# Kernel optimization log

Hardware: AMD Instinct MI355X
Metric: run time of the kernel (lower is better)

Reference implementation:

```python
import jax, jax.numpy as jnp
import numpy as np

B, S, D = 2, 2048, 4096
QH, KVH = 32, 8
HD = D // QH          # 128
KVD = KVH * HD        # 1024
GROUP = QH // KVH     # 4


def _make_freqs_cis(seq, hd):
    inv = 1.0 / (10000.0 ** (jnp.arange(0, hd, 2, dtype=jnp.float32) / hd))
    ang = jnp.outer(jnp.arange(seq, dtype=jnp.float32), inv)  # [S, HD//2]
    return jnp.stack([jnp.cos(ang), jnp.sin(ang)], axis=-1)    # [S, HD//2, 2]


def setup_inputs() -> dict:
    key = jax.random.key(0)
    ks = jax.random.split(key, 10)
    std = 0.02
    return {
        "xs": jax.random.normal(ks[0], (B, S, D), jnp.float32),
        "startpos": 0,
        "freqs_cis": _make_freqs_cis(S, HD),
        "Wq": jax.random.normal(ks[1], (D, D), jnp.float32) * std,
        "bq": jnp.zeros((D,), jnp.float32),
        "Wk": jax.random.normal(ks[2], (KVD, D), jnp.float32) * std,
        "bk": jnp.zeros((KVD,), jnp.float32),
        "Wv": jax.random.normal(ks[3], (KVD, D), jnp.float32) * std,
        "bv": jnp.zeros((KVD,), jnp.float32),
        "Wo": jax.random.normal(ks[4], (D, D), jnp.float32) * std,
        "bo": jnp.zeros((D,), jnp.float32),
    }


def _apply_rope(x, fc):
    # x: [B,S,H,HD], fc: [S, HD//2, 2] (cos,sin) -> complex multiply per pair
    xr = x.reshape(*x.shape[:-1], HD // 2, 2)
    cos = fc[None, :, None, :, 0]
    sin = fc[None, :, None, :, 1]
    out_r = xr[..., 0] * cos - xr[..., 1] * sin
    out_i = xr[..., 0] * sin + xr[..., 1] * cos
    return jnp.stack([out_r, out_i], axis=-1).reshape(x.shape)


def reference(xs, startpos, freqs_cis, Wq, bq, Wk, bk, Wv, bv, Wo, bo):
    b, s, _ = xs.shape
    q = (xs @ Wq.T + bq).reshape(b, s, QH, HD)
    k = (xs @ Wk.T + bk).reshape(b, s, KVH, HD)
    v = (xs @ Wv.T + bv).reshape(b, s, KVH, HD)

    fc = freqs_cis[startpos:startpos + s]
    q = _apply_rope(q, fc)
    k = _apply_rope(k, fc)
    # startpos == 0: cache write-then-read is identity on current k/v

    # GQA: group q heads per kv head; avoid materializing repeated K/V
    qg = q.transpose(0, 2, 1, 3).reshape(b, KVH, GROUP, s, HD)  # [b,kvh,g,s,d]
    kk = k.transpose(0, 2, 1, 3)                                 # [b,kvh,t,d]
    vv = v.transpose(0, 2, 1, 3)

    scale = 1.0 / jnp.sqrt(jnp.float32(HD))
    logits = jnp.einsum('bhgsd,bhtd->bhgst', qg, kk) * scale
    causal = jnp.tril(jnp.ones((s, s), dtype=bool))
    logits = jnp.where(causal[None, None, None], logits, jnp.float32(-1e30))
    probs = jax.nn.softmax(logits, axis=-1)
    ctx = jnp.einsum('bhgst,bhtd->bhgsd', probs, vv)             # [b,kvh,g,s,d]

    ctx = ctx.reshape(b, QH, s, HD).transpose(0, 2, 1, 3).reshape(b, s, D)
    return ctx @ Wo.T + bo
```

## Files before the change

### kernel.cpp

```cpp
#include <hip/hip_runtime.h>
#include <hip/hip_bf16.h>

typedef __bf16 bf16x8 __attribute__((ext_vector_type(8)));
typedef float  f32x4  __attribute__((ext_vector_type(4)));

#define MFMA(a, b, c) __builtin_amdgcn_mfma_f32_16x16x32_bf16((a), (b), (c), 0, 0, 0)

typedef __attribute__((address_space(1))) void* as1_vp;
typedef __attribute__((address_space(3))) void* as3_vp;

__device__ __forceinline__ void g2lds16(const void* g, void* lds) {
  __builtin_amdgcn_global_load_lds((as1_vp)(unsigned long long)g,
                                   (as3_vp)(unsigned int)(unsigned long long)lds,
                                   16, 0, 0);
}

__device__ __forceinline__ unsigned short bfbits(float x) {
  return __builtin_bit_cast(unsigned short, __float2bfloat16(x));
}

__global__ void cvt_f32_bf16(const float* __restrict__ in,
                             __hip_bfloat16* __restrict__ out, int n4) {
  int i = blockIdx.x * blockDim.x + threadIdx.x;
  if (i >= n4) return;
  float4 v = ((const float4*)in)[i];
  ushort4 u;
  u.x = bfbits(v.x); u.y = bfbits(v.y); u.z = bfbits(v.z); u.w = bfbits(v.w);
  ((ushort4*)out)[i] = u;
}

__global__ void concat_bias(const float* __restrict__ bq, const float* __restrict__ bk,
                            const float* __restrict__ bv, float* __restrict__ out) {
  int i = blockIdx.x * 256 + threadIdx.x;
  float v = (i < 4096) ? bq[i] : ((i < 5120) ? bk[i - 4096] : bv[i - 5120]);
  out[i] = v;
}

__global__ void rope_inplace(__hip_bfloat16* __restrict__ x, const float* __restrict__ fc,
                             const int* __restrict__ startpos, int pitch, int wshift,
                             long npairs) {
  long i = (long)blockIdx.x * blockDim.x + threadIdx.x;
  if (i >= npairs) return;
  int  wi    = (int)(i & ((1 << wshift) - 1));
  long token = i >> wshift;
  int  s  = (int)(token & 2047);
  int  j  = wi & 63;
  int  sp = startpos[0] + s;
  float c  = fc[(sp << 7) + (j << 1)];
  float sn = fc[(sp << 7) + (j << 1) + 1];
  long base = token * pitch + wi * 2;
  float xr = __bfloat162float(x[base]);
  float xi = __bfloat162float(x[base + 1]);
  x[base]     = __float2bfloat16(xr * c - xi * sn);
  x[base + 1] = __float2bfloat16(xr * sn + xi * c);
}

__global__ void transpose_v(const __hip_bfloat16* __restrict__ QKV,
                            __hip_bfloat16* __restrict__ VT) {
  __shared__ __hip_bfloat16 tile[32][33];
  int z = blockIdx.z, b = z >> 3, kvh = z & 7;
  int s0 = blockIdx.x * 32, h0 = blockIdx.y * 32;
  int tx = threadIdx.x, ty = threadIdx.y;
#pragma unroll
  for (int ry = ty; ry < 32; ry += 8)
    tile[ry][tx] =
        QKV[(long)(b * 2048 + s0 + ry) * 6144 + 5120 + kvh * 128 + h0 + tx];
  __syncthreads();
#pragma unroll
  for (int ry = ty; ry < 32; ry += 8)
    VT[((long)z * 128 + h0 + ry) * 2048 + s0 + tx] = tile[tx][ry];
}

#define BAR()  __builtin_amdgcn_s_barrier()
#define SB0()  __builtin_amdgcn_sched_barrier(0)
#define LGK0() do { asm volatile("s_waitcnt lgkmcnt(0)" ::: "memory"); \
                    __builtin_amdgcn_sched_barrier(0); } while (0)
#define VMC8() asm volatile("s_waitcnt vmcnt(8)" ::: "memory")
#define VMC4() asm volatile("s_waitcnt vmcnt(4)" ::: "memory")
#define VMC0() asm volatile("s_waitcnt vmcnt(0)" ::: "memory")
#define PRI1() __builtin_amdgcn_s_setprio(1)
#define PRI0() __builtin_amdgcn_s_setprio(0)

template <int OUT_F32>
__global__ void __launch_bounds__(512, 2)
gemm256_bt(const __hip_bfloat16* __restrict__ A,
           const __hip_bfloat16* __restrict__ W,
           const float* __restrict__ bias,
           void* __restrict__ Cout, int M, int N, int K) {
  __shared__ __align__(16) char smem[131072];
  (void)M;
  const int t = threadIdx.x, w = t >> 6, l = t & 63, quad = l >> 4, lan = l & 15;
  const int wm = w >> 2, wn = w & 3;

  const int nwg = gridDim.x;
  const int xcd = blockIdx.x & 7, lid = blockIdx.x >> 3;
  const int qq = nwg >> 3, rr = nwg & 7;
  const int wg = (xcd < rr ? xcd * (qq + 1) : rr * (qq + 1) + (xcd - rr) * qq) + lid;
  const int ntn = N >> 8;
  const int bm = (wg / ntn) << 8, bn = (wg % ntn) << 8;

  const int csrc = ((t & 3) ^ ((t >> 3) & 3)) << 4;
  const char* aS0 = (const char*)(A + (long)(bm + (t >> 2)) * K) + csrc;
  const char* aS1 = aS0 + (long)K * 256;
  const char* bS0 = (const char*)(W + (long)(bn + (t >> 2)) * K) + csrc;
  const char* bS1 = bS0 + (long)K * 256;
  char* dA0 = smem + (w << 10);
  char* dA1 = smem + 16384 + (w << 10);
  char* dB0 = smem + 32768 + (w << 10);
  char* dB1 = smem + 49152 + (w << 10);

#define STG(src, dst, kt, bb)                                    \
  g2lds16((src) + (kt) * 128, (dst) + (bb) * 65536);             \
  g2lds16((src) + (kt) * 128 + 64, (dst) + (bb) * 65536 + 8192);

  const int rsw = (quad ^ ((lan >> 1) & 3)) << 4;
  const char* aR = smem + wm * 16384 + (lan << 6) + rsw;
  const char* bR = smem + 32768 + (wn >> 1) * 16384 + ((((wn & 1) << 6) + lan) << 6) + rsw;

  f32x4 acc[8][4] = {};
  bf16x8 fA[4][2], fB0[2][2], fB1[2][2];

#define RD_A(mb, bb)                                                          \
  _Pragma("unroll") for (int mm = 0; mm < 4; ++mm)                            \
  _Pragma("unroll") for (int j = 0; j < 2; ++j)                               \
    fA[mm][j] = *(const bf16x8*)(aR + (bb) * 65536 + ((mb) + mm) * 1024 + j * 8192);
#define RD_B(arr, nb, bb)                                                     \
  _Pragma("unroll") for (int nn = 0; nn < 2; ++nn)                            \
  _Pragma("unroll") for (int j = 0; j < 2; ++j)                               \
    arr[nn][j] = *(const bf16x8*)(bR + (bb) * 65536 + ((nb) + nn) * 1024 + j * 8192);
#define MM16(mb, arr, nb)                                                     \
  _Pragma("unroll") for (int mm = 0; mm < 4; ++mm)                            \
  _Pragma("unroll") for (int nn = 0; nn < 2; ++nn)                            \
  _Pragma("unroll") for (int j = 0; j < 2; ++j)                               \
    acc[(mb) + mm][(nb) + nn] = MFMA(fA[mm][j], arr[nn][j], acc[(mb) + mm][(nb) + nn]);

  STG(aS0, dA0, 0, 0); STG(aS1, dA1, 0, 0);
  STG(bS0, dB0, 0, 0); STG(bS1, dB1, 0, 0);
  STG(bS0, dB0, 1, 1); STG(bS1, dB1, 1, 1);
  VMC4();
  BAR();

  const int NT = K >> 6;
  for (int i = 0; i < (NT >> 1) - 1; ++i) {
    const int t0 = i << 1;
    RD_A(0, 0); RD_B(fB0, 0, 0);
    STG(aS0, dA0, t0 + 1, 1);
    SB0(); BAR(); LGK0();
    PRI1(); MM16(0, fB0, 0); PRI0();
    BAR();
    RD_B(fB1, 2, 0);
    STG(aS1, dA1, t0 + 1, 1);
    SB0(); BAR(); LGK0();
    PRI1(); MM16(0, fB1, 2); PRI0();
    BAR();
    RD_A(4, 0);
    STG(bS0, dB0, t0 + 2, 0);
    SB0(); BAR(); LGK0();
    PRI1(); MM16(4, fB0, 0); PRI0();
    BAR();
    STG(bS1, dB1, t0 + 2, 0);
    SB0(); BAR();
    PRI1(); MM16(4, fB1, 2); PRI0();
    VMC4();
    BAR();
    RD_A(0, 1); RD_B(fB0, 0, 1);
    STG(aS0, dA0, t0 + 2, 0);
    SB0(); BAR(); LGK0();
    PRI1(); MM16(0, fB0, 0); PRI0();
    BAR();
    RD_B(fB1, 2, 1);
    STG(aS1, dA1, t0 + 2, 0);
    SB0(); BAR(); LGK0();
    PRI1(); MM16(0, fB1, 2); PRI0();
    BAR();
    RD_A(4, 1);
    STG(bS0, dB0, t0 + 3, 1);
    SB0(); BAR(); LGK0();
    PRI1(); MM16(4, fB0, 0); PRI0();
    BAR();
    STG(bS1, dB1, t0 + 3, 1);
    SB0(); BAR();
    PRI1(); MM16(4, fB1, 2); PRI0();
    VMC4();
    BAR();
  }

  {
    RD_A(0, 0); RD_B(fB0, 0, 0);
    STG(aS0, dA0, NT - 1, 1);
    SB0(); BAR(); LGK0();
    PRI1(); MM16(0, fB0, 0); PRI0();
    BAR();
    RD_B(fB1, 2, 0);
    STG(aS1, dA1, NT - 1, 1);
    SB0(); BAR(); LGK0();
    PRI1(); MM16(0, fB1, 2); PRI0();
    BAR();
    RD_A(4, 0);
    SB0(); BAR(); LGK0();
    PRI1(); MM16(4, fB0, 0); PRI0();
    BAR();
    BAR();
    PRI1(); MM16(4, fB1, 2); PRI0();
    VMC0();
    BAR();
    RD_A(0, 1); RD_B(fB0, 0, 1);
    SB0(); BAR(); LGK0();
    PRI1(); MM16(0, fB0, 0); PRI0();
    BAR();
    RD_B(fB1, 2, 1);
    SB0(); BAR(); LGK0();
    PRI1(); MM16(0, fB1, 2); PRI0();
    BAR();
    RD_A(4, 1);
    SB0(); BAR(); LGK0();
    PRI1(); MM16(4, fB0, 0); PRI0();
    BAR();
    PRI1(); MM16(4, fB1, 2); PRI0();
  }

  float bsv[4];
#pragma unroll
  for (int n = 0; n < 4; ++n) bsv[n] = bias[bn + (wn << 6) + (n << 4) + lan];
#pragma unroll
  for (int m = 0; m < 8; ++m) {
#pragma unroll
    for (int e = 0; e < 4; ++e) {
      const long row = bm + (wm << 7) + (m << 4) + (quad << 2) + e;
#pragma unroll
      for (int n = 0; n < 4; ++n) {
        const float v = acc[m][n][e] + bsv[n];
        const long col = bn + (wn << 6) + (n << 4) + lan;
        if (OUT_F32) ((float*)Cout)[row * N + col] = v;
        else ((__hip_bfloat16*)Cout)[row * N + col] = __float2bfloat16(v);
      }
    }
  }
}
#undef STG
#undef RD_A
#undef RD_B
#undef MM16

__global__ void __launch_bounds__(256, 2) flash_attn(const __hip_bfloat16* __restrict__ QKV,
                                                     const __hip_bfloat16* __restrict__ VT,
                                                     __hip_bfloat16* __restrict__ Ctx, int S) {
  __shared__ __align__(16) char smem[66560];
  char* Ks0 = smem;
  char* Ks1 = smem + 16384;
  char* Vs  = smem + 32768;
  char* Ps  = smem + 49152;
  const int t = threadIdx.x, w = t >> 6, l = t & 63, quad = l >> 4, lan = l & 15;
  const int b = blockIdx.z, qh = blockIdx.y, kvh = qh >> 2;
  const int q0idx = (int)gridDim.x - 1 - blockIdx.x;
  const int q0 = q0idx << 7;
  const float cl = 0.08838834764831845f * 1.4426950408889634f;

  {
    int rl = l >> 4, cd = l & 15;
#pragma unroll
    for (int ii = 0; ii < 8; ii++) {
      int i = (w << 3) + ii;
      int r = (i << 2) + rl;
      int cs = cd ^ (r & 15);
      const char* g =
          (const char*)(QKV + (long)(b * S + q0 + r) * 6144 + qh * 128) + (cs << 4);
      g2lds16(g, smem + (i << 10));
    }
  }
  __syncthreads();
  bf16x8 qf[2][4];
#pragma unroll
  for (int st = 0; st < 2; st++) {
    int row = ((((w << 1) + st) << 4) + lan);
#pragma unroll
    for (int ks = 0; ks < 4; ks++)
      qf[st][ks] = *(const bf16x8*)(smem + (row << 8) + ((((ks << 2) + quad) ^ lan) << 4));
  }
  __syncthreads();

  const int ntiles = (q0idx << 1) + 2;

  auto stageK = [&](int kt, char* dst) {
    int rl = l >> 4, cd = l & 15;
#pragma unroll
    for (int ii = 0; ii < 4; ii++) {
      int i = (w << 2) + ii;
      int r = (i << 2) + rl;
      int cs = cd ^ (r & 15);
      const char* g =
          (const char*)(QKV + (long)(b * S + (kt << 6) + r) * 6144 + 4096 + kvh * 128) +
          (cs << 4);
      g2lds16(g, dst + (i << 10));
    }
  };
  auto stageV = [&](int kt) {
    int dl = l >> 3, cd2 = l & 7;
#pragma unroll
    for (int ii = 0; ii < 4; ii++) {
      int i = (w << 2) + ii;
      int d = (i << 3) + dl;
      int cs = cd2 ^ dl;
      const char* g =
          (const char*)(VT + ((long)((b << 3) + kvh) * 128 + d) * S + (kt << 6)) + (cs << 4);
      g2lds16(g, Vs + (i << 10));
    }
  };

  f32x4 o[2][8] = {};
  float m0[2] = {-__builtin_inff(), -__builtin_inff()};
  float lsum[2] = {0.f, 0.f};

  stageK(0, Ks0);

  for (int kt = 0; kt < ntiles; kt++) {
    const int t0 = kt << 6;
    char* Kcur = (kt & 1) ? Ks1 : Ks0;
    char* Knxt = (kt & 1) ? Ks0 : Ks1;
    SB0(); BAR();
    stageV(kt);
    const int tn = (kt + 1 < ntiles) ? kt + 1 : kt;
    stageK(tn, Knxt);
    VMC8();
    SB0(); BAR();

    f32x4 sa[2][4] = {{}, {}};
    PRI1();
#pragma unroll
    for (int j = 0; j < 4; j++)
#pragma unroll
      for (int ks = 0; ks < 4; ks++) {
        bf16x8 kf = *(const bf16x8*)(Kcur + (((j << 4) + lan) << 8) +
                                     ((((ks << 2) + quad) ^ lan) << 4));
        sa[0][j] = MFMA(kf, qf[0][ks], sa[0][j]);
        sa[1][j] = MFMA(kf, qf[1][ks], sa[1][j]);
      }
    PRI0();

#pragma unroll
    for (int st = 0; st < 2; st++) {
      const int strip = (w << 1) + st;
      const int qg = q0 + (strip << 4) + lan;
      if (t0 + 63 > q0 + (strip << 4)) {
#pragma unroll
        for (int j = 0; j < 4; j++)
#pragma unroll
          for (int e = 0; e < 4; e++)
            if (t0 + (j << 4) + (quad << 2) + e > qg) sa[st][j][e] = -1e30f;
      }
      float mq = sa[st][0][0];
#pragma unroll
      for (int j = 0; j < 4; j++)
#pragma unroll
        for (int e = 0; e < 4; e++) mq = fmaxf(mq, sa[st][j][e]);
      mq = fmaxf(mq, __shfl_xor(mq, 16));
      mq = fmaxf(mq, __shfl_xor(mq, 32));
      float mn = fmaxf(m0[st], mq);
      float al = exp2f((m0[st] - mn) * cl);
      m0[st] = mn;
      float rs = 0.f;
      char* prow = Ps + strip * 2176 + lan * 136;
#pragma unroll
      for (int j = 0; j < 4; j++) {
        float p0 = exp2f((sa[st][j][0] - mn) * cl);
        float p1 = exp2f((sa[st][j][1] - mn) * cl);
        float p2 = exp2f((sa[st][j][2] - mn) * cl);
        float p3 = exp2f((sa[st][j][3] - mn) * cl);
        rs += (p0 + p1) + (p2 + p3);
        ushort4 u;
        u.x = bfbits(p0); u.y = bfbits(p1); u.z = bfbits(p2); u.w = bfbits(p3);
        *(ushort4*)(prow + (j << 5) + (quad << 3)) = u;
      }
      rs += __shfl_xor(rs, 16);
      rs += __shfl_xor(rs, 32);
      lsum[st] = lsum[st] * al + rs;
#pragma unroll
      for (int dt = 0; dt < 8; dt++) o[st][dt] *= al;
    }

    bf16x8 pf[2][2];
#pragma unroll
    for (int st = 0; st < 2; st++) {
      char* prow = Ps + ((w << 1) + st) * 2176 + lan * 136;
      pf[st][0] = *(const bf16x8*)(prow + (quad << 4));
      pf[st][1] = *(const bf16x8*)(prow + 64 + (quad << 4));
    }

    VMC4();
    SB0(); BAR();

    PRI1();
#pragma unroll
    for (int dt = 0; dt < 8; dt++) {
      const int drow = (dt << 4) + lan;
#pragma unroll
      for (int ks = 0; ks < 2; ks++) {
        bf16x8 vf = *(const bf16x8*)(Vs + (drow << 7) +
                                     ((((ks << 2) + quad) ^ (lan & 7)) << 4));
        o[0][dt] = MFMA(vf, pf[0][ks], o[0][dt]);
        o[1][dt] = MFMA(vf, pf[1][ks], o[1][dt]);
      }
    }
    PRI0();
  }

#pragma unroll
  for (int st = 0; st < 2; st++) {
    float inv = 1.0f / lsum[st];
    int strip = (w << 1) + st;
    long token = (long)b * S + q0 + (strip << 4) + lan;
    __hip_bfloat16* obase = Ctx + token * 4096 + qh * 128;
#pragma unroll
    for (int dt = 0; dt < 8; dt++) {
      ushort4 u;
      u.x = bfbits(o[st][dt][0] * inv);
      u.y = bfbits(o[st][dt][1] * inv);
      u.z = bfbits(o[st][dt][2] * inv);
      u.w = bfbits(o[st][dt][3] * inv);
      *(ushort4*)(obase + (dt << 4) + (quad << 2)) = u;
    }
  }
}

extern "C" void kernel_launch(void* const* d_in, const int* in_sizes, int n_in,
                              void* d_out, int out_size, void* d_ws, size_t ws_size,
                              hipStream_t stream) {
  const float* xs = (const float*)d_in[0];
  const int* startpos = (const int*)d_in[1];
  const float* fc = (const float*)d_in[2];
  const float* Wq = (const float*)d_in[3];
  const float* bq = (const float*)d_in[4];
  const float* Wk = (const float*)d_in[5];
  const float* bk = (const float*)d_in[6];
  const float* Wv = (const float*)d_in[7];
  const float* bv = (const float*)d_in[8];
  const float* Wo = (const float*)d_in[9];
  const float* bo = (const float*)d_in[10];
  float* out = (float*)d_out;
  char* ws = (char*)d_ws;

  __hip_bfloat16* Wqkvb = (__hip_bfloat16*)(ws);
  __hip_bfloat16* Xb    = (__hip_bfloat16*)(ws + 50331648L);
  __hip_bfloat16* QKVb  = (__hip_bfloat16*)(ws + 83886080L);
  __hip_bfloat16* VbT   = (__hip_bfloat16*)(ws + 134217728L);
  float*          bqkv  = (float*)(ws + 142606336L);
  __hip_bfloat16* Wob   = Wqkvb;
  __hip_bfloat16* Ctx   = Xb;

  cvt_f32_bf16<<<16384, 256, 0, stream>>>(xs, Xb, 4194304);
  cvt_f32_bf16<<<16384, 256, 0, stream>>>(Wq, Wqkvb, 4194304);
  cvt_f32_bf16<<<4096, 256, 0, stream>>>(Wk, Wqkvb + 16777216L, 1048576);
  cvt_f32_bf16<<<4096, 256, 0, stream>>>(Wv, Wqkvb + 20971520L, 1048576);
  concat_bias<<<24, 256, 0, stream>>>(bq, bk, bv, bqkv);

  gemm256_bt<0><<<dim3(384), 512, 0, stream>>>(Xb, Wqkvb, bqkv, QKVb, 4096, 6144, 4096);

  rope_inplace<<<32768, 256, 0, stream>>>(QKVb, fc, startpos, 6144, 11, 8388608L);
  rope_inplace<<<8192, 256, 0, stream>>>(QKVb + 4096, fc, startpos, 6144, 9, 2097152L);
  transpose_v<<<dim3(64, 4, 16), dim3(32, 8), 0, stream>>>(QKVb, VbT);
  cvt_f32_bf16<<<16384, 256, 0, stream>>>(Wo, Wob, 4194304);

  flash_attn<<<dim3(16, 32, 2), 256, 0, stream>>>(QKVb, VbT, Ctx, 2048);

  gemm256_bt<1><<<dim3(256), 512, 0, stream>>>(Ctx, Wob, bo, out, 4096, 4096, 4096);
}
```

Measured before the change: 808.9 us.

## Keep softmax probabilities in registers for PV MFMA and add lazy rescaling

The P tile no longer round-trips through LDS. The probabilities stay in registers as bf16 packs and feed 16x16x16 MFMAs directly, with V^T pre-permuted in the transpose kernel so its LDS fragment layout matches the score accumulator layout. The online-softmax rescale of the output and row sum is skipped unless the running max grows past a threshold, and bf16 packing uses v_cvt_pk_bf16_f32. This removes LDS writes and reads, and cuts LDS from 66560 to 49152 bytes, at the cost of twice as many smaller MFMAs for PV and a looser softmax max bound.

```diff
diff --git a/kernel.cpp b/kernel.cpp
--- a/kernel.cpp
+++ b/kernel.cpp
@@ -3,8 +3,10 @@
 
 typedef __bf16 bf16x8 __attribute__((ext_vector_type(8)));
 typedef float  f32x4  __attribute__((ext_vector_type(4)));
+typedef short  s16x4  __attribute__((ext_vector_type(4)));
 
 #define MFMA(a, b, c) __builtin_amdgcn_mfma_f32_16x16x32_bf16((a), (b), (c), 0, 0, 0)
+#define MFMA16(a, b, c) __builtin_amdgcn_mfma_f32_16x16x16bf16_1k((a), (b), (c), 0, 0, 0)
 
 typedef __attribute__((address_space(1))) void* as1_vp;
 typedef __attribute__((address_space(3))) void* as3_vp;
@@ -17,6 +19,12 @@
 
 __device__ __forceinline__ unsigned short bfbits(float x) {
   return __builtin_bit_cast(unsigned short, __float2bfloat16(x));
+}
+
+__device__ __forceinline__ unsigned cvtpk(float a, float b) {
+  unsigned r;
+  asm("v_cvt_pk_bf16_f32 %0, %1, %2" : "=v"(r) : "v"(a), "v"(b));
+  return r;
 }
 
 __global__ void cvt_f32_bf16(const float* __restrict__ in,
@@ -24,9 +32,10 @@
   int i = blockIdx.x * blockDim.x + threadIdx.x;
   if (i >= n4) return;
   float4 v = ((const float4*)in)[i];
-  ushort4 u;
-  u.x = bfbits(v.x); u.y = bfbits(v.y); u.z = bfbits(v.z); u.w = bfbits(v.w);
-  ((ushort4*)out)[i] = u;
+  uint2 u;
+  u.x = cvtpk(v.x, v.y);
+  u.y = cvtpk(v.z, v.w);
+  ((uint2*)out)[i] = u;
 }
 
 __global__ void concat_bias(const float* __restrict__ bq, const float* __restrict__ bk,
@@ -67,8 +76,11 @@
         QKV[(long)(b * 2048 + s0 + ry) * 6144 + 5120 + kvh * 128 + h0 + tx];
   __syncthreads();
 #pragma unroll
-  for (int ry = ty; ry < 32; ry += 8)
-    VT[((long)z * 128 + h0 + ry) * 2048 + s0 + tx] = tile[tx][ry];
+  for (int ry = ty; ry < 32; ry += 8) {
+    int dd = h0 + ry;
+    int tc = (s0 + tx) ^ (((dd >> 3) & 1) << 2);
+    VT[((long)z * 128 + dd) * 2048 + tc] = tile[tx][ry];
+  }
 }
 
 #define BAR()  __builtin_amdgcn_s_barrier()
@@ -245,11 +257,10 @@
 __global__ void __launch_bounds__(256, 2) flash_attn(const __hip_bfloat16* __restrict__ QKV,
                                                      const __hip_bfloat16* __restrict__ VT,
                                                      __hip_bfloat16* __restrict__ Ctx, int S) {
-  __shared__ __align__(16) char smem[66560];
+  __shared__ __align__(16) char smem[49152];
   char* Ks0 = smem;
   char* Ks1 = smem + 16384;
   char* Vs  = smem + 32768;
-  char* Ps  = smem + 49152;
   const int t = threadIdx.x, w = t >> 6, l = t & 63, quad = l >> 4, lan = l & 15;
   const int b = blockIdx.z, qh = blockIdx.y, kvh = qh >> 2;
   const int q0idx = (int)gridDim.x - 1 - blockIdx.x;
@@ -310,6 +321,9 @@
   f32x4 o[2][8] = {};
   float m0[2] = {-__builtin_inff(), -__builtin_inff()};
   float lsum[2] = {0.f, 0.f};
+
+  const int l7 = lan & 7;
+  const int hb = (quad & 1) ^ ((lan >> 3) & 1);
 
   stageK(0, Ks0);
 
@@ -337,6 +351,7 @@
       }
     PRI0();
 
+    s16x4 pb[2][4];
 #pragma unroll
     for (int st = 0; st < 2; st++) {
       const int strip = (w << 1) + st;
@@ -355,35 +370,31 @@
         for (int e = 0; e < 4; e++) mq = fmaxf(mq, sa[st][j][e]);
       mq = fmaxf(mq, __shfl_xor(mq, 16));
       mq = fmaxf(mq, __shfl_xor(mq, 32));
-      float mn = fmaxf(m0[st], mq);
-      float al = exp2f((m0[st] - mn) * cl);
-      m0[st] = mn;
+      if (__any(mq > m0[st] + 62.0f)) {
+        float mn = fmaxf(m0[st], mq);
+        float al = exp2f((m0[st] - mn) * cl);
+        m0[st] = mn;
+        lsum[st] *= al;
+#pragma unroll
+        for (int dt = 0; dt < 8; dt++) o[st][dt] *= al;
+      }
+      float nm = -m0[st] * cl;
       float rs = 0.f;
-      char* prow = Ps + strip * 2176 + lan * 136;
 #pragma unroll
       for (int j = 0; j < 4; j++) {
-        float p0 = exp2f((sa[st][j][0] - mn) * cl);
-        float p1 = exp2f((sa[st][j][1] - mn) * cl);
-        float p2 = exp2f((sa[st][j][2] - mn) * cl);
-        float p3 = exp2f((sa[st][j][3] - mn) * cl);
+        float p0 = exp2f(fmaf(sa[st][j][0], cl, nm));
+        float p1 = exp2f(fmaf(sa[st][j][1], cl, nm));
+        float p2 = exp2f(fmaf(sa[st][j][2], cl, nm));
+        float p3 = exp2f(fmaf(sa[st][j][3], cl, nm));
         rs += (p0 + p1) + (p2 + p3);
-        ushort4 u;
-        u.x = bfbits(p0); u.y = bfbits(p1); u.z = bfbits(p2); u.w = bfbits(p3);
-        *(ushort4*)(prow + (j << 5) + (quad << 3)) = u;
+        uint2 up;
+        up.x = cvtpk(p0, p1);
+        up.y = cvtpk(p2, p3);
+        pb[st][j] = __builtin_bit_cast(s16x4, up);
       }
       rs += __shfl_xor(rs, 16);
       rs += __shfl_xor(rs, 32);
-      lsum[st] = lsum[st] * al + rs;
-#pragma unroll
-      for (int dt = 0; dt < 8; dt++) o[st][dt] *= al;
-    }
-
-    bf16x8 pf[2][2];
-#pragma unroll
-    for (int st = 0; st < 2; st++) {
-      char* prow = Ps + ((w << 1) + st) * 2176 + lan * 136;
-      pf[st][0] = *(const bf16x8*)(prow + (quad << 4));
-      pf[st][1] = *(const bf16x8*)(prow + 64 + (quad << 4));
+      lsum[st] += rs;
     }
 
     VMC4();
@@ -393,12 +404,12 @@
 #pragma unroll
     for (int dt = 0; dt < 8; dt++) {
       const int drow = (dt << 4) + lan;
-#pragma unroll
-      for (int ks = 0; ks < 2; ks++) {
-        bf16x8 vf = *(const bf16x8*)(Vs + (drow << 7) +
-                                     ((((ks << 2) + quad) ^ (lan & 7)) << 4));
-        o[0][dt] = MFMA(vf, pf[0][ks], o[0][dt]);
-        o[1][dt] = MFMA(vf, pf[1][ks], o[1][dt]);
+      const char* vbase = Vs + (drow << 7) + (hb << 3);
+#pragma unroll
+      for (int j = 0; j < 4; j++) {
+        s16x4 vf = *(const s16x4*)(vbase + ((((j << 1) + (quad >> 1)) ^ l7) << 4));
+        o[0][dt] = MFMA16(vf, pb[0][j], o[0][dt]);
+        o[1][dt] = MFMA16(vf, pb[1][j], o[1][dt]);
       }
     }
     PRI0();
@@ -412,12 +423,10 @@
     __hip_bfloat16* obase = Ctx + token * 4096 + qh * 128;
 #pragma unroll
     for (int dt = 0; dt < 8; dt++) {
-      ushort4 u;
-      u.x = bfbits(o[st][dt][0] * inv);
-      u.y = bfbits(o[st][dt][1] * inv);
-      u.z = bfbits(o[st][dt][2] * inv);
-      u.w = bfbits(o[st][dt][3] * inv);
-      *(ushort4*)(obase + (dt << 4) + (quad << 2)) = u;
+      uint2 u;
+      u.x = cvtpk(o[st][dt][0] * inv, o[st][dt][1] * inv);
+      u.y = cvtpk(o[st][dt][2] * inv, o[st][dt][3] * inv);
+      *(uint2*)(obase + (dt << 4) + (quad << 2)) = u;
     }
   }
 }
```

New measurement: 779.0 us. 1.04x faster.
